# Kernel optimization log

Hardware: AMD Instinct MI355X
Metric: run time of the kernel (lower is better)

Reference implementation:

```python
import jax, jax.numpy as jnp
import numpy as np

V, E, HID, K, S = 100000, 256, 512, 20, 4096
HD = HID // 2  # per-direction LSTM hidden
START_ID, STOP_ID = 18, 19


def setup_inputs() -> dict:
    key = jax.random.key(0)
    ks = jax.random.split(key, 14)
    sentence = jax.random.randint(ks[0], (S,), 0, V)
    tags = jax.random.randint(ks[1], (S,), 0, START_ID)  # real tags only
    embed = jax.random.normal(ks[2], (V, E), jnp.float32) * 0.1
    w_ih_f = jax.random.normal(ks[3], (4 * HD, E), jnp.float32) * 0.05
    w_hh_f = jax.random.normal(ks[4], (4 * HD, HD), jnp.float32) * 0.05
    b_f = jax.random.normal(ks[5], (4 * HD,), jnp.float32) * 0.05
    w_ih_b = jax.random.normal(ks[6], (4 * HD, E), jnp.float32) * 0.05
    w_hh_b = jax.random.normal(ks[7], (4 * HD, HD), jnp.float32) * 0.05
    b_b = jax.random.normal(ks[8], (4 * HD,), jnp.float32) * 0.05
    h0 = jax.random.normal(ks[9], (2, HD), jnp.float32)
    c0 = jax.random.normal(ks[10], (2, HD), jnp.float32)
    emit_W = jax.random.normal(ks[11], (K, HID), jnp.float32) * 0.05
    emit_b = jax.random.normal(ks[12], (K,), jnp.float32) * 0.05
    transition = jax.random.normal(ks[13], (K, K), jnp.float32)
    transition = transition.at[START_ID, :].set(-10000.0)
    transition = transition.at[:, STOP_ID].set(-10000.0)
    return dict(sentence=sentence, tags=tags, embed=embed,
                w_ih_f=w_ih_f, w_hh_f=w_hh_f, b_f=b_f,
                w_ih_b=w_ih_b, w_hh_b=w_hh_b, b_b=b_b,
                h0=h0, c0=c0, emit_W=emit_W, emit_b=emit_b,
                transition=transition)


def _lstm_scan(xs, w_ih, w_hh, b, h, c):
    # xs: (S, E); torch gate order i, f, g, o
    def step(carry, x):
        h, c = carry
        z = x @ w_ih.T + h @ w_hh.T + b  # (4*HD,)
        i, f, g, o = jnp.split(z, 4)
        i, f, o = jax.nn.sigmoid(i), jax.nn.sigmoid(f), jax.nn.sigmoid(o)
        g = jnp.tanh(g)
        c = f * c + i * g
        h = o * jnp.tanh(c)
        return (h, c), h
    _, hs = jax.lax.scan(step, (h, c), xs)
    return hs  # (S, HD)


def reference(sentence, tags, embed, w_ih_f, w_hh_f, b_f,
              w_ih_b, w_hh_b, b_b, h0, c0, emit_W, emit_b, transition):
    xs = embed[sentence]  # (S, E)
    h_fwd = _lstm_scan(xs, w_ih_f, w_hh_f, b_f, h0[0], c0[0])
    h_bwd = _lstm_scan(xs[::-1], w_ih_b, w_hh_b, b_b, h0[1], c0[1])[::-1]
    feats = jnp.concatenate([h_fwd, h_bwd], axis=-1) @ emit_W.T + emit_b  # (S, K)

    # CRF forward algorithm (log-partition), tag dim fully vectorized.
    init_fv = jnp.full((K,), -10000.0, feats.dtype).at[START_ID].set(0.0)

    def crf_step(fv, feat):
        # fv_new[next] = logsumexp_prev(fv[prev] + T[next, prev] + feat[next])
        fv = jax.scipy.special.logsumexp(fv[None, :] + transition + feat[:, None], axis=1)
        return fv, None

    fv, _ = jax.lax.scan(crf_step, init_fv, feats)
    log_z = jax.scipy.special.logsumexp(fv + transition[STOP_ID])

    # Gold path score.
    tags_ext = jnp.concatenate([jnp.array([START_ID], tags.dtype), tags])
    gold = (transition[tags_ext[1:], tags_ext[:-1]].sum()
            + feats[jnp.arange(S), tags].sum()
            + transition[STOP_ID, tags[-1]])
    return jnp.stack([log_z, gold])
```

## Files before the change

### kernel.cpp

```cpp
#include <hip/hip_runtime.h>
#include <stdint.h>

#define SLEN 4096
#define EDIM 256
#define HD 256
#define G4 1024
#define KT 20
#define START_ID 18
#define STOP_ID 19

#define NLC 9
#define LSTM_LDS_BYTES (1024 + 1024 * NLC * 16)

typedef _Float16 half_t;
typedef _Float16 half2_t __attribute__((ext_vector_type(2)));

__device__ __forceinline__ float dot2(uint32_t w, uint32_t h, float acc) {
#if __has_builtin(__builtin_amdgcn_fdot2)
    return __builtin_amdgcn_fdot2(__builtin_bit_cast(half2_t, w),
                                  __builtin_bit_cast(half2_t, h), acc, false);
#else
    half2_t wv = __builtin_bit_cast(half2_t, w);
    half2_t hv = __builtin_bit_cast(half2_t, h);
    acc += (float)wv.x * (float)hv.x;
    acc += (float)wv.y * (float)hv.y;
    return acc;
#endif
}

__device__ __forceinline__ float fsig(float x) { return 1.f / (1.f + __expf(-x)); }
__device__ __forceinline__ float ftanh(float x) { return 1.f - 2.f / (__expf(2.f * x) + 1.f); }


__global__ __launch_bounds__(256) void k_transpose_ih(const float* __restrict__ wf,
                                                      const float* __restrict__ wb,
                                                      float* __restrict__ wT) {
    __shared__ float tile[32][33];
    int d = blockIdx.z;
    const float* w = d ? wb : wf;
    int ob = blockIdx.x * 32;
    int eb = blockIdx.y * 32;
    int tx = threadIdx.x & 31, ty = threadIdx.x >> 5;
#pragma unroll
    for (int r = 0; r < 32; r += 8)
        tile[ty + r][tx] = w[(long)(ob + ty + r) * EDIM + eb + tx];
    __syncthreads();
    float* dst = wT + (long)d * EDIM * G4;
#pragma unroll
    for (int r = 0; r < 32; r += 8)
        dst[(long)(eb + ty + r) * G4 + ob + tx] = tile[tx][ty + r];
}

__global__ __launch_bounds__(1024) void k_pack_hh(const float* __restrict__ whf,
                                                  const float* __restrict__ whb,
                                                  uint32_t* __restrict__ wpack,
                                                  uint32_t* __restrict__ wtail) {
    int d = blockIdx.y;
    const float* W = d ? whb : whf;
    int t = threadIdx.x;
    int l = t & 63;
    int w = t >> 6;
    int kh = l >> 5;
    int gA = (l >> 4) & 1;
    int j = (w << 4) | (l & 15);
    int rowA = gA * 256 + j;
    int rowB = (gA + 2) * 256 + j;
    int bx = blockIdx.x;

    auto packdw = [&](int dd) -> uint32_t {
        int cc = dd >> 2, qq = dd & 3;
        int row = (cc < 16) ? rowA : rowB;
        int k = kh * 128 + (cc & 15) * 8 + qq * 2;
        half2_t p = {(half_t)W[(long)row * HD + k], (half_t)W[(long)row * HD + k + 1]};
        return __builtin_bit_cast(uint32_t, p);
    };

    if (bx < 92) {
        wpack[(d * 92 + bx) * 1024 + t] = packdw(bx);
    } else {
        int cb = bx - 92;
        uint4* dst = (uint4*)wtail;
        dst[(d * NLC + cb) * 1024 + t] = make_uint4(packdw(92 + cb * 4), packdw(93 + cb * 4),
                                                    packdw(94 + cb * 4), packdw(95 + cb * 4));
    }
}

__global__ __launch_bounds__(256) void k_zx(const int* __restrict__ sentence,
                                            const float* __restrict__ embed,
                                            const float* __restrict__ wT,
                                            const float* __restrict__ bf,
                                            const float* __restrict__ bb,
                                            float* __restrict__ zxp) {
    int d = blockIdx.y;
    int s0 = blockIdx.x * 16;
    const float* bias = d ? bb : bf;
    __shared__ float xbuf[16][EDIM];
    int tid = threadIdx.x;
    for (int r = 0; r < 16; r++) {
        int row = sentence[s0 + r];
        xbuf[r][tid] = embed[(long)row * EDIM + tid];
    }
    __syncthreads();
    const float* wTd = wT + (long)d * EDIM * G4;
    for (int og = 0; og < 4; og++) {
        float acc[16];
#pragma unroll
        for (int r = 0; r < 16; r++) acc[r] = 0.f;
        int o = og * 256 + tid;
        for (int e = 0; e < EDIM; e += 4) {
            float w0 = wTd[(long)(e + 0) * G4 + o];
            float w1 = wTd[(long)(e + 1) * G4 + o];
            float w2 = wTd[(long)(e + 2) * G4 + o];
            float w3 = wTd[(long)(e + 3) * G4 + o];
#pragma unroll
            for (int r = 0; r < 16; r++) {
                float4 x4 = *(const float4*)&xbuf[r][e];
                acc[r] += w0 * x4.x + w1 * x4.y + w2 * x4.z + w3 * x4.w;
            }
        }
        float bv = bias[o];
        int tB = ((tid >> 4) << 6) | (og << 4) | (tid & 15);
#pragma unroll
        for (int r = 0; r < 16; r++)
            zxp[(long)(d * SLEN + s0 + r) * G4 + tB] = acc[r] + bv;
    }
}

__global__ __launch_bounds__(1024, 4) void k_lstm(const float* __restrict__ zxp,
                                                  const uint32_t* __restrict__ wpack,
                                                  const uint4* __restrict__ wtail,
                                                  const float* __restrict__ h0,
                                                  const float* __restrict__ c0,
                                                  float* __restrict__ hs) {
    extern __shared__ char smem[];
    uint4* h2q = (uint4*)smem;
    half_t* h2h = (half_t*)smem;
    uint4* tail = (uint4*)(smem + 1024);

    int d = blockIdx.x;
    int t = threadIdx.x;
    int l = t & 63;
    int w = t >> 6;
    int kh = l >> 5;
    int gA = (l >> 4) & 1;
    int lj = l & 15;
    int j = (w << 4) | lj;

    uint32_t wreg[92];
#pragma unroll
    for (int kk = 0; kk < 92; kk++) wreg[kk] = wpack[(d * 92 + kk) * 1024 + t];

#pragma unroll
    for (int cb = 0; cb < NLC; cb++)
        tail[cb * 1024 + t] = wtail[(d * NLC + cb) * 1024 + t];

    float c = c0[d * HD + j];
    if (t < 128) {
        half2_t p = {(half_t)h0[d * HD + 2 * t], (half_t)h0[d * HD + 2 * t + 1]};
        ((uint32_t*)h2q)[t] = __builtin_bit_cast(uint32_t, p);
    }
    __syncthreads();

    const float* zxd = zxp + (long)d * SLEN * G4;
    float* hsd = hs + (long)d * SLEN * HD + j;
    int colA = (w << 6) | (gA << 4) | lj;

    int sx0 = d ? (SLEN - 1) : 0;
    float zxAn = zxd[(long)sx0 * G4 + colA];
    float zxBn = zxd[(long)sx0 * G4 + colA + 32];

    for (int s = 0; s < SLEN; s++) {
        const int p = s & 1;
        float zxA = zxAn, zxB = zxBn;
        if (s + 1 < SLEN) {
            int sxn = d ? (SLEN - 2 - s) : (s + 1);
            zxAn = zxd[(long)sxn * G4 + colA];
            zxBn = zxd[(long)sxn * G4 + colA + 32];
        }

        const uint4* hq = h2q + p * 32 + kh * 16;
        float pA0 = 0.f, pA1 = 0.f, pB0 = 0.f, pB1 = 0.f;
#pragma unroll
        for (int cc = 0; cc < 16; cc++) {
            uint4 hv = hq[cc];
            pA0 = dot2(wreg[4 * cc + 0], hv.x, pA0);
            pA1 = dot2(wreg[4 * cc + 1], hv.y, pA1);
            pA0 = dot2(wreg[4 * cc + 2], hv.z, pA0);
            pA1 = dot2(wreg[4 * cc + 3], hv.w, pA1);
            if (cc < 7) {
                pB0 = dot2(wreg[64 + 4 * cc + 0], hv.x, pB0);
                pB1 = dot2(wreg[64 + 4 * cc + 1], hv.y, pB1);
                pB0 = dot2(wreg[64 + 4 * cc + 2], hv.z, pB0);
                pB1 = dot2(wreg[64 + 4 * cc + 3], hv.w, pB1);
            } else {
                uint4 tw = tail[(cc - 7) * 1024 + t];
                pB0 = dot2(tw.x, hv.x, pB0);
                pB1 = dot2(tw.y, hv.y, pB1);
                pB0 = dot2(tw.z, hv.z, pB0);
                pB1 = dot2(tw.w, hv.w, pB1);
            }
        }

        float sA = pA0 + pA1;
        float sB = pB0 + pB1;
        sA += __shfl_xor(sA, 32, 64);
        sB += __shfl_xor(sB, 32, 64);
        float zAf = sA + zxA;
        float zBf = sB + zxB;

        float zi = __shfl(zAf, lj, 64);
        float zf = __shfl(zAf, lj + 16, 64);
        float zg = __shfl(zBf, lj, 64);
        float zo = __shfl(zBf, lj + 16, 64);

        float ig = fsig(zi), fg = fsig(zf), og = fsig(zo);
        float gg = ftanh(zg);
        c = fg * c + ig * gg;
        float hval = og * ftanh(c);
        if (l < 16) {
            int sx = d ? (SLEN - 1 - s) : s;
            hsd[(long)sx * HD] = hval;
            h2h[((p ^ 1) << 8) + j] = (half_t)hval;
        }
        __syncthreads();
    }
}

__global__ __launch_bounds__(192) void k_feats(const float* __restrict__ hs,
                                               const float* __restrict__ emitW,
                                               const float* __restrict__ emitb,
                                               float* __restrict__ feats) {
    __shared__ float wb[KT][516];
    __shared__ float hb[8][516];
    int tid = threadIdx.x;
    int s0 = blockIdx.x * 8;
    for (int idx = tid; idx < KT * 512; idx += 192) {
        wb[idx >> 9][idx & 511] = emitW[idx];
    }
    for (int idx = tid; idx < 8 * 512; idx += 192) {
        int sl = idx >> 9, jj = idx & 511;
        float v = (jj < 256) ? hs[(long)(s0 + sl) * HD + jj]
                             : hs[(long)(SLEN + s0 + sl) * HD + (jj - 256)];
        hb[sl][jj] = v;
    }
    __syncthreads();
    if (tid < 160) {
        int sl = tid / KT, k = tid % KT;
        float acc = emitb[k];
        for (int jj = 0; jj < 512; jj += 4) {
            float4 wv = *(const float4*)&wb[k][jj];
            float4 hv = *(const float4*)&hb[sl][jj];
            acc += wv.x * hv.x + wv.y * hv.y + wv.z * hv.z + wv.w * hv.w;
        }
        feats[(long)(s0 + sl) * KT + k] = acc;
    }
}

__global__ __launch_bounds__(256) void k_gold(const float* __restrict__ feats,
                                              const int* __restrict__ tags,
                                              const float* __restrict__ trans,
                                              float* __restrict__ out) {
    __shared__ float red[256];
    int tid = threadIdx.x;
    float local = 0.f;
    for (int s2 = tid; s2 < SLEN; s2 += 256) {
        int cur = tags[s2];
        int prev = s2 ? tags[s2 - 1] : START_ID;
        local += trans[cur * KT + prev] + feats[(long)s2 * KT + cur];
    }
    red[tid] = local;
    __syncthreads();
    for (int off = 128; off; off >>= 1) {
        if (tid < off) red[tid] += red[tid + off];
        __syncthreads();
    }
    if (tid == 0) out[1] = red[0] + trans[STOP_ID * KT + tags[SLEN - 1]];
}

__global__ __launch_bounds__(512) void k_crf_chunk(const float* __restrict__ feats,
                                                   const float* __restrict__ trans,
                                                   float* __restrict__ mats) {
    __shared__ float T[KT][KT + 1];
    __shared__ float fb[16][KT];
    __shared__ float cur[2][KT][KT + 1];
    int tid = threadIdx.x;
    int t0 = blockIdx.x * 16;
    if (tid < KT * KT) T[tid / KT][tid % KT] = trans[tid];
    for (int idx = tid; idx < 16 * KT; idx += 512) fb[idx / KT][idx % KT] = feats[(long)t0 * KT + idx];
    __syncthreads();
    int i = tid / KT, jc = tid % KT;
    bool act = tid < KT * KT;
    if (act) cur[0][i][jc] = T[i][jc] + fb[0][i];
    __syncthreads();
    for (int m = 1; m < 16; m++) {
        int p = (m - 1) & 1;
        float nv = 0.f;
        if (act) {
            float vs[KT], vmax = -1e30f;
#pragma unroll
            for (int k = 0; k < KT; k++) { vs[k] = T[i][k] + cur[p][k][jc]; vmax = fmaxf(vmax, vs[k]); }
            float sum = 0.f;
#pragma unroll
            for (int k = 0; k < KT; k++) sum += __expf(vs[k] - vmax);
            nv = fb[m][i] + vmax + __logf(sum);
        }
        if (act) cur[p ^ 1][i][jc] = nv;
        __syncthreads();
    }
    if (act) mats[(long)blockIdx.x * (KT * KT) + tid] = cur[1][i][jc];
}

__global__ __launch_bounds__(512) void k_crf_combine(const float* __restrict__ in,
                                                     float* __restrict__ out_mats,
                                                     int per_block,
                                                     const float* __restrict__ trans,
                                                     float* __restrict__ d_out_ptr,
                                                     int finalize) {
    __shared__ float A[KT][KT + 1];
    __shared__ float cur[2][KT][KT + 1];
    int tid = threadIdx.x;
    int b = blockIdx.x;
    int i = tid / KT, jc = tid % KT;
    bool act = tid < KT * KT;
    const float* base = in + (long)b * per_block * (KT * KT);
    if (act) cur[0][i][jc] = base[tid];
    __syncthreads();
    for (int m = 1; m < per_block; m++) {
        int p = (m - 1) & 1;
        if (act) A[i][jc] = base[(long)m * KT * KT + tid];
        __syncthreads();
        float nv = 0.f;
        if (act) {
            float vs[KT], vmax = -1e30f;
#pragma unroll
            for (int k = 0; k < KT; k++) { vs[k] = A[i][k] + cur[p][k][jc]; vmax = fmaxf(vmax, vs[k]); }
            float sum = 0.f;
#pragma unroll
            for (int k = 0; k < KT; k++) sum += __expf(vs[k] - vmax);
            nv = vmax + __logf(sum);
        }
        if (act) cur[p ^ 1][i][jc] = nv;
        __syncthreads();
    }
    int fbuf = (per_block - 1) & 1;
    if (!finalize) {
        if (act) out_mats[(long)b * KT * KT + tid] = cur[fbuf][i][jc];
        return;
    }
    if (tid == 0) {
        float fv[KT];
        for (int ii = 0; ii < KT; ii++) {
            float vs[KT], vmax = -1e30f;
            for (int k = 0; k < KT; k++) {
                float v = cur[fbuf][ii][k] + (k == START_ID ? 0.f : -10000.f);
                vs[k] = v;
                vmax = fmaxf(vmax, v);
            }
            float sum = 0.f;
            for (int k = 0; k < KT; k++) sum += __expf(vs[k] - vmax);
            fv[ii] = vmax + __logf(sum);
        }
        float vs2[KT], vmax = -1e30f;
        for (int ii = 0; ii < KT; ii++) {
            float v = fv[ii] + trans[STOP_ID * KT + ii];
            vs2[ii] = v;
            vmax = fmaxf(vmax, v);
        }
        float sum = 0.f;
        for (int ii = 0; ii < KT; ii++) sum += __expf(vs2[ii] - vmax);
        d_out_ptr[0] = vmax + __logf(sum);
    }
}

extern "C" void kernel_launch(void* const* d_in, const int* in_sizes, int n_in,
                              void* d_out, int out_size, void* d_ws, size_t ws_size,
                              hipStream_t stream) {
    const int* sentence = (const int*)d_in[0];
    const int* tags = (const int*)d_in[1];
    const float* embed = (const float*)d_in[2];
    const float* w_ih_f = (const float*)d_in[3];
    const float* w_hh_f = (const float*)d_in[4];
    const float* b_f = (const float*)d_in[5];
    const float* w_ih_b = (const float*)d_in[6];
    const float* w_hh_b = (const float*)d_in[7];
    const float* b_b = (const float*)d_in[8];
    const float* h0 = (const float*)d_in[9];
    const float* c0 = (const float*)d_in[10];
    const float* emit_W = (const float*)d_in[11];
    const float* emit_b = (const float*)d_in[12];
    const float* transition = (const float*)d_in[13];
    float* out = (float*)d_out;

    char* ws = (char*)d_ws;
    float* zxp = (float*)(ws + 0);
    float* hs = (float*)(ws + 33554432);
    float* wT = (float*)(ws + 41943040);
    uint32_t* wpack = (uint32_t*)(ws + 44040192);
    uint32_t* wtail = (uint32_t*)(ws + 44793856);
    float* feats = (float*)(ws + 45088768);
    float* mats = (float*)(ws + 45416448);
    float* mats2 = (float*)(ws + 45826048);

    (void)hipFuncSetAttribute((const void*)k_lstm,
                              hipFuncAttributeMaxDynamicSharedMemorySize,
                              LSTM_LDS_BYTES);

    k_transpose_ih<<<dim3(32, 8, 2), 256, 0, stream>>>(w_ih_f, w_ih_b, wT);
    k_pack_hh<<<dim3(101, 2), 1024, 0, stream>>>(w_hh_f, w_hh_b, wpack, wtail);
    k_zx<<<dim3(256, 2), 256, 0, stream>>>(sentence, embed, wT, b_f, b_b, zxp);
    k_lstm<<<dim3(2), 1024, LSTM_LDS_BYTES, stream>>>(zxp, wpack, (const uint4*)wtail, h0, c0, hs);
    k_feats<<<dim3(512), 192, 0, stream>>>(hs, emit_W, emit_b, feats);
    k_gold<<<dim3(1), 256, 0, stream>>>(feats, tags, transition, out);
    k_crf_chunk<<<dim3(256), 512, 0, stream>>>(feats, transition, mats);
    k_crf_combine<<<dim3(16), 512, 0, stream>>>(mats, mats2, 16, transition, out, 0);
    k_crf_combine<<<dim3(1), 512, 0, stream>>>(mats2, nullptr, 16, transition, out, 1);
}
```

Baseline: 8.573 ms.

## Repartition LSTM recurrent matvec so each lane computes all four gates

Each lane now handles one hidden unit's four gates over a quarter of K, instead of two gate rows over half of K. The four gate pre-activations are reduced with two xor-shuffles, which removes the gate-gather shuffles. The h buffer is padded per K-quarter to avoid LDS bank conflicts. The input-projection kernel writes all four gates per unit as a float4 so the recurrent loop loads zx with one vector load. This trades extra reduction shuffles and a padded LDS layout for fewer dependent shuffles and fewer global loads per step.

```diff
diff --git a/kernel.cpp b/kernel.cpp
--- a/kernel.cpp
+++ b/kernel.cpp
@@ -10,7 +10,9 @@
 #define STOP_ID 19
 
 #define NLC 9
-#define LSTM_LDS_BYTES (1024 + 1024 * NLC * 16)
+#define HPAD 144
+#define HBUF (4 * HPAD)
+#define LSTM_LDS_BYTES (2048 + 1024 * NLC * 16)
 
 typedef _Float16 half_t;
 typedef _Float16 half2_t __attribute__((ext_vector_type(2)));
@@ -60,17 +62,15 @@
     int t = threadIdx.x;
     int l = t & 63;
     int w = t >> 6;
-    int kh = l >> 5;
-    int gA = (l >> 4) & 1;
+    int kq = l >> 4;
     int j = (w << 4) | (l & 15);
-    int rowA = gA * 256 + j;
-    int rowB = (gA + 2) * 256 + j;
     int bx = blockIdx.x;
 
     auto packdw = [&](int dd) -> uint32_t {
         int cc = dd >> 2, qq = dd & 3;
-        int row = (cc < 16) ? rowA : rowB;
-        int k = kh * 128 + (cc & 15) * 8 + qq * 2;
+        int gate = cc >> 3;
+        int row = gate * 256 + j;
+        int k = kq * 64 + (cc & 7) * 8 + qq * 2;
         half2_t p = {(half_t)W[(long)row * HD + k], (half_t)W[(long)row * HD + k + 1]};
         return __builtin_bit_cast(uint32_t, p);
     };
@@ -95,35 +95,42 @@
     int s0 = blockIdx.x * 16;
     const float* bias = d ? bb : bf;
     __shared__ float xbuf[16][EDIM];
-    int tid = threadIdx.x;
+    int u = threadIdx.x;
     for (int r = 0; r < 16; r++) {
         int row = sentence[s0 + r];
-        xbuf[r][tid] = embed[(long)row * EDIM + tid];
+        xbuf[r][u] = embed[(long)row * EDIM + u];
     }
     __syncthreads();
     const float* wTd = wT + (long)d * EDIM * G4;
-    for (int og = 0; og < 4; og++) {
-        float acc[16];
-#pragma unroll
-        for (int r = 0; r < 16; r++) acc[r] = 0.f;
-        int o = og * 256 + tid;
-        for (int e = 0; e < EDIM; e += 4) {
-            float w0 = wTd[(long)(e + 0) * G4 + o];
-            float w1 = wTd[(long)(e + 1) * G4 + o];
-            float w2 = wTd[(long)(e + 2) * G4 + o];
-            float w3 = wTd[(long)(e + 3) * G4 + o];
-#pragma unroll
-            for (int r = 0; r < 16; r++) {
-                float4 x4 = *(const float4*)&xbuf[r][e];
-                acc[r] += w0 * x4.x + w1 * x4.y + w2 * x4.z + w3 * x4.w;
+    float4 a[16];
+    float4 bv = make_float4(bias[u], bias[256 + u], bias[512 + u], bias[768 + u]);
+#pragma unroll
+    for (int r = 0; r < 16; r++) a[r] = bv;
+    for (int e = 0; e < EDIM; e += 4) {
+        float w0[4], w1[4], w2[4], w3[4];
+#pragma unroll
+        for (int k = 0; k < 4; k++) {
+            w0[k] = wTd[(long)(e + k) * G4 + u];
+            w1[k] = wTd[(long)(e + k) * G4 + 256 + u];
+            w2[k] = wTd[(long)(e + k) * G4 + 512 + u];
+            w3[k] = wTd[(long)(e + k) * G4 + 768 + u];
+        }
+#pragma unroll
+        for (int r = 0; r < 16; r++) {
+            float4 x4 = *(const float4*)&xbuf[r][e];
+            float xv[4] = {x4.x, x4.y, x4.z, x4.w};
+#pragma unroll
+            for (int k = 0; k < 4; k++) {
+                a[r].x += w0[k] * xv[k];
+                a[r].y += w1[k] * xv[k];
+                a[r].z += w2[k] * xv[k];
+                a[r].w += w3[k] * xv[k];
             }
         }
-        float bv = bias[o];
-        int tB = ((tid >> 4) << 6) | (og << 4) | (tid & 15);
-#pragma unroll
-        for (int r = 0; r < 16; r++)
-            zxp[(long)(d * SLEN + s0 + r) * G4 + tB] = acc[r] + bv;
-    }
+    }
+#pragma unroll
+    for (int r = 0; r < 16; r++)
+        *(float4*)&zxp[(long)(d * SLEN + s0 + r) * G4 + u * 4] = a[r];
 }
 
 __global__ __launch_bounds__(1024, 4) void k_lstm(const float* __restrict__ zxp,
@@ -133,16 +140,14 @@
                                                   const float* __restrict__ c0,
                                                   float* __restrict__ hs) {
     extern __shared__ char smem[];
-    uint4* h2q = (uint4*)smem;
-    half_t* h2h = (half_t*)smem;
-    uint4* tail = (uint4*)(smem + 1024);
+    char* hbase = smem;
+    uint4* tail = (uint4*)(smem + 2048);
 
     int d = blockIdx.x;
     int t = threadIdx.x;
     int l = t & 63;
     int w = t >> 6;
-    int kh = l >> 5;
-    int gA = (l >> 4) & 1;
+    int kq = l >> 4;
     int lj = l & 15;
     int j = (w << 4) | lj;
 
@@ -156,62 +161,69 @@
 
     float c = c0[d * HD + j];
     if (t < 128) {
-        half2_t p = {(half_t)h0[d * HD + 2 * t], (half_t)h0[d * HD + 2 * t + 1]};
-        ((uint32_t*)h2q)[t] = __builtin_bit_cast(uint32_t, p);
+        int u2 = 2 * t;
+        half2_t p = {(half_t)h0[d * HD + u2], (half_t)h0[d * HD + u2 + 1]};
+        *(uint32_t*)(hbase + (u2 >> 6) * HPAD + (u2 & 63) * 2) = __builtin_bit_cast(uint32_t, p);
     }
     __syncthreads();
 
     const float* zxd = zxp + (long)d * SLEN * G4;
     float* hsd = hs + (long)d * SLEN * HD + j;
-    int colA = (w << 6) | (gA << 4) | lj;
 
     int sx0 = d ? (SLEN - 1) : 0;
-    float zxAn = zxd[(long)sx0 * G4 + colA];
-    float zxBn = zxd[(long)sx0 * G4 + colA + 32];
+    float4 zxn = *(const float4*)&zxd[(long)sx0 * G4 + j * 4];
 
     for (int s = 0; s < SLEN; s++) {
         const int p = s & 1;
-        float zxA = zxAn, zxB = zxBn;
+        float4 zx = zxn;
         if (s + 1 < SLEN) {
             int sxn = d ? (SLEN - 2 - s) : (s + 1);
-            zxAn = zxd[(long)sxn * G4 + colA];
-            zxBn = zxd[(long)sxn * G4 + colA + 32];
-        }
-
-        const uint4* hq = h2q + p * 32 + kh * 16;
-        float pA0 = 0.f, pA1 = 0.f, pB0 = 0.f, pB1 = 0.f;
-#pragma unroll
-        for (int cc = 0; cc < 16; cc++) {
+            zxn = *(const float4*)&zxd[(long)sxn * G4 + j * 4];
+        }
+
+        const uint4* hq = (const uint4*)(hbase + p * HBUF + kq * HPAD);
+        float aI0 = 0.f, aI1 = 0.f, aF0 = 0.f, aF1 = 0.f;
+        float aG0 = 0.f, aG1 = 0.f, aO0 = 0.f, aO1 = 0.f;
+#pragma unroll
+        for (int cc = 0; cc < 8; cc++) {
             uint4 hv = hq[cc];
-            pA0 = dot2(wreg[4 * cc + 0], hv.x, pA0);
-            pA1 = dot2(wreg[4 * cc + 1], hv.y, pA1);
-            pA0 = dot2(wreg[4 * cc + 2], hv.z, pA0);
-            pA1 = dot2(wreg[4 * cc + 3], hv.w, pA1);
+            aI0 = dot2(wreg[4 * cc + 0], hv.x, aI0);
+            aI1 = dot2(wreg[4 * cc + 1], hv.y, aI1);
+            aI0 = dot2(wreg[4 * cc + 2], hv.z, aI0);
+            aI1 = dot2(wreg[4 * cc + 3], hv.w, aI1);
+            aF0 = dot2(wreg[32 + 4 * cc + 0], hv.x, aF0);
+            aF1 = dot2(wreg[32 + 4 * cc + 1], hv.y, aF1);
+            aF0 = dot2(wreg[32 + 4 * cc + 2], hv.z, aF0);
+            aF1 = dot2(wreg[32 + 4 * cc + 3], hv.w, aF1);
             if (cc < 7) {
-                pB0 = dot2(wreg[64 + 4 * cc + 0], hv.x, pB0);
-                pB1 = dot2(wreg[64 + 4 * cc + 1], hv.y, pB1);
-                pB0 = dot2(wreg[64 + 4 * cc + 2], hv.z, pB0);
-                pB1 = dot2(wreg[64 + 4 * cc + 3], hv.w, pB1);
+                aG0 = dot2(wreg[64 + 4 * cc + 0], hv.x, aG0);
+                aG1 = dot2(wreg[64 + 4 * cc + 1], hv.y, aG1);
+                aG0 = dot2(wreg[64 + 4 * cc + 2], hv.z, aG0);
+                aG1 = dot2(wreg[64 + 4 * cc + 3], hv.w, aG1);
             } else {
-                uint4 tw = tail[(cc - 7) * 1024 + t];
-                pB0 = dot2(tw.x, hv.x, pB0);
-                pB1 = dot2(tw.y, hv.y, pB1);
-                pB0 = dot2(tw.z, hv.z, pB0);
-                pB1 = dot2(tw.w, hv.w, pB1);
+                uint4 tw = tail[t];
+                aG0 = dot2(tw.x, hv.x, aG0);
+                aG1 = dot2(tw.y, hv.y, aG1);
+                aG0 = dot2(tw.z, hv.z, aG0);
+                aG1 = dot2(tw.w, hv.w, aG1);
             }
-        }
-
-        float sA = pA0 + pA1;
-        float sB = pB0 + pB1;
-        sA += __shfl_xor(sA, 32, 64);
-        sB += __shfl_xor(sB, 32, 64);
-        float zAf = sA + zxA;
-        float zBf = sB + zxB;
-
-        float zi = __shfl(zAf, lj, 64);
-        float zf = __shfl(zAf, lj + 16, 64);
-        float zg = __shfl(zBf, lj, 64);
-        float zo = __shfl(zBf, lj + 16, 64);
+            uint4 ow = tail[(1 + cc) * 1024 + t];
+            aO0 = dot2(ow.x, hv.x, aO0);
+            aO1 = dot2(ow.y, hv.y, aO1);
+            aO0 = dot2(ow.z, hv.z, aO0);
+            aO1 = dot2(ow.w, hv.w, aO1);
+        }
+
+        float zi = aI0 + aI1, zf = aF0 + aF1, zg = aG0 + aG1, zo = aO0 + aO1;
+        zi += __shfl_xor(zi, 16, 64);
+        zf += __shfl_xor(zf, 16, 64);
+        zg += __shfl_xor(zg, 16, 64);
+        zo += __shfl_xor(zo, 16, 64);
+        zi += __shfl_xor(zi, 32, 64);
+        zf += __shfl_xor(zf, 32, 64);
+        zg += __shfl_xor(zg, 32, 64);
+        zo += __shfl_xor(zo, 32, 64);
+        zi += zx.x; zf += zx.y; zg += zx.z; zo += zx.w;
 
         float ig = fsig(zi), fg = fsig(zf), og = fsig(zo);
         float gg = ftanh(zg);
@@ -220,7 +232,7 @@
         if (l < 16) {
             int sx = d ? (SLEN - 1 - s) : s;
             hsd[(long)sx * HD] = hval;
-            h2h[((p ^ 1) << 8) + j] = (half_t)hval;
+            *(half_t*)(hbase + (p ^ 1) * HBUF + (j >> 6) * HPAD + (j & 63) * 2) = (half_t)hval;
         }
         __syncthreads();
     }
```

Result: slower. 9.095 ms (+6.1%).
